# Kernel tuning notes

Measured on AMD Instinct MI355X. Metric: run time of the kernel, lower is better.

## Reference

```python
import jax, jax.numpy as jnp
import numpy as np

EPS = 1e-6
B, C, D = 128, 1000, 1024


def setup_inputs() -> dict:
    key = jax.random.key(0)
    k1, k2, k3, k4 = jax.random.split(key, 4)
    x = jax.random.normal(k1, (B, D), dtype=jnp.float32)
    # xavier-normal-ish prototypes
    mu = jax.random.normal(k2, (C, D), dtype=jnp.float32) * (2.0 / (C + D)) ** 0.5
    beta = jax.random.normal(k3, (D,), dtype=jnp.float32) * 0.1
    # L initialized as identity + small lower-triangular noise (full_sigma=True)
    L = jnp.eye(D, dtype=jnp.float32) + jnp.tril(
        jax.random.normal(k4, (D, D), dtype=jnp.float32) * 0.01)
    lmbda = jnp.asarray(0.1, dtype=jnp.float32)
    scale = jnp.asarray(10.0, dtype=jnp.float32)
    return {"x": x, "mu": mu, "beta": beta, "L": L, "lmbda": lmbda, "scale": scale}


def reference(x, mu, beta, L, lmbda, scale):
    # Sigma = tril(L) @ tril(L)^T + eps*I  (positive definite)
    Lt = jnp.tril(L)
    sigma = Lt @ Lt.T + EPS * jnp.eye(L.shape[0], dtype=L.dtype)
    # diff: [B, C, D]
    diff = x[:, None, :] - mu[None, :, :]
    # quadratic form v^T Sigma v per (b, c): contract once, then reduce
    ds = jnp.einsum('bcd,df->bcf', diff, sigma)   # [B, C, D]
    quad = jnp.sum(ds * diff, axis=-1)            # [B, C]
    beta_dot = jnp.einsum('d,bcd->bc', beta, diff)  # [B, C]
    riemannian = jnp.sqrt(quad + EPS)
    directional = lmbda * jnp.sqrt(beta_dot * beta_dot + EPS)  # smooth |.|
    return -scale * (riemannian + directional)
```

## Files before the change

### kernel.cpp

```cpp
#include <hip/hip_runtime.h>

#define D_DIM 1024
#define B_DIM 128
#define C_DIM 1000
#define M_ALL 1152
#define EPSF 1e-6f

typedef __attribute__((ext_vector_type(8))) short short8;
typedef __attribute__((ext_vector_type(4))) float f32x4;

static __device__ __forceinline__ unsigned short f2bf(float f) {
    union { float f; unsigned int u; } v; v.f = f;
    unsigned int u = v.u;
    u += 0x7fffu + ((u >> 16) & 1u);
    return (unsigned short)(u >> 16);
}


__global__ __launch_bounds__(256)
void pack_all(const float* __restrict__ x, const float* __restrict__ mu,
              const float* __restrict__ beta, const float* __restrict__ L,
              unsigned short* __restrict__ A_frag, unsigned short* __restrict__ LT_frag,
              float* __restrict__ nrm, float* __restrict__ bdot) {
    __shared__ __align__(16) unsigned short s_tile[64 * 72];
    __shared__ float red[2][4];
    const int tid = threadIdx.x, bid = blockIdx.x;

    if (bid < M_ALL) {
        const int m = bid;
        float4 v;
        if (m < B_DIM)              v = *(const float4*)(x + m * D_DIM + tid * 4);
        else if (m < B_DIM + C_DIM) v = *(const float4*)(mu + (m - B_DIM) * D_DIM + tid * 4);
        else                        v = make_float4(0.f, 0.f, 0.f, 0.f);
        ushort4 o;
        o.x = f2bf(v.x); o.y = f2bf(v.y); o.z = f2bf(v.z); o.w = f2bf(v.w);
        int mtile = m >> 4, kc = tid >> 3, qk = (tid >> 1) & 3, jj = (tid & 1) * 4;
        *(ushort4*)(A_frag + (mtile * 32 + kc) * 512 + (qk * 16 + (m & 15)) * 8 + jj) = o;

        float4 bt4 = *(const float4*)(beta + tid * 4);
        float sa = v.x*v.x + v.y*v.y + v.z*v.z + v.w*v.w;
        float sb = bt4.x*v.x + bt4.y*v.y + bt4.z*v.z + bt4.w*v.w;
#pragma unroll
        for (int off = 32; off > 0; off >>= 1) {
            sa += __shfl_down(sa, off);
            sb += __shfl_down(sb, off);
        }
        int lane = tid & 63, wv = tid >> 6;
        if (lane == 0) { red[0][wv] = sa; red[1][wv] = sb; }
        __syncthreads();
        if (tid == 0) {
            nrm[m]  = EPSF * (red[0][0] + red[0][1] + red[0][2] + red[0][3]);
            bdot[m] = red[1][0] + red[1][1] + red[1][2] + red[1][3];
        }
    } else {
        const int t = bid - M_ALL;
        const int k0 = (t >> 4) * 64, n0 = (t & 15) * 64;
        const int tn = tid & 63, tq = tid >> 6;
#pragma unroll
        for (int i = 0; i < 16; ++i) {
            int kk = tq + i * 4;
            int k = k0 + kk, n = n0 + tn;
            float v = (k >= n) ? L[k * D_DIM + n] : 0.f;
            s_tile[tn * 72 + kk] = f2bf(v);
        }
        __syncthreads();
        const int p = tid >> 5, s = tid & 31;
        const int np = p >> 1, kc2 = p & 1;
        const int ntile = (n0 >> 4) + np, kcg = (k0 >> 5) + kc2;
#pragma unroll
        for (int e = 0; e < 2; ++e) {
            int l = s * 2 + e;
            int lq = l >> 4, nr = l & 15;
            short8 vv = *(const short8*)&s_tile[(np * 16 + nr) * 72 + kc2 * 32 + lq * 8];
            *(short8*)(LT_frag + (ntile * 32 + kcg) * 512 + l * 8) = vv;
        }
    }
}

__global__ __launch_bounds__(256)
void gemm_p(const unsigned short* __restrict__ A_frag,
            const unsigned short* __restrict__ LT_frag,
            unsigned short* __restrict__ P_frag, float* __restrict__ nrm) {
    __shared__ __align__(16) unsigned short s_resh[4 * 1024];
    const int wv = threadIdx.x >> 6, lane = threadIdx.x & 63;
    const int wid = blockIdx.x * 4 + wv;
    const int lrow = lane & 15, q = lane >> 4;
    const int mt = wid >> 5, nt = wid & 31;
    const unsigned short* Ab0 = A_frag  + ((2 * mt) * 32) * 512 + lane * 8;
    const unsigned short* Ab1 = Ab0 + 32 * 512;
    const unsigned short* Bb0 = LT_frag + ((2 * nt) * 32) * 512 + lane * 8;
    const unsigned short* Bb1 = Bb0 + 32 * 512;

    f32x4 acc[2][2] = {};
#pragma unroll 4
    for (int kc = nt; kc < 32; ++kc) {
        short8 a0 = *(const short8*)(Ab0 + kc * 512);
        short8 a1 = *(const short8*)(Ab1 + kc * 512);
        short8 b0 = *(const short8*)(Bb0 + kc * 512);
        short8 b1 = *(const short8*)(Bb1 + kc * 512);
        acc[0][0] = __builtin_amdgcn_mfma_f32_16x16x32_bf16(a0, b0, acc[0][0], 0, 0, 0);
        acc[0][1] = __builtin_amdgcn_mfma_f32_16x16x32_bf16(a0, b1, acc[0][1], 0, 0, 0);
        acc[1][0] = __builtin_amdgcn_mfma_f32_16x16x32_bf16(a1, b0, acc[1][0], 0, 0, 0);
        acc[1][1] = __builtin_amdgcn_mfma_f32_16x16x32_bf16(a1, b1, acc[1][1], 0, 0, 0);
    }

#pragma unroll
    for (int mi = 0; mi < 2; ++mi)
#pragma unroll
    for (int r = 0; r < 4; ++r) {
        float s = acc[mi][0][r] * acc[mi][0][r] + acc[mi][1][r] * acc[mi][1][r];
#pragma unroll
        for (int off = 1; off < 16; off <<= 1) s += __shfl_xor(s, off);
        if (lrow == 0) atomicAdd(&nrm[mt * 32 + mi * 16 + q * 4 + r], s);
    }
    unsigned short* wls = s_resh + wv * 1024;
#pragma unroll
    for (int mi = 0; mi < 2; ++mi)
#pragma unroll
    for (int ni = 0; ni < 2; ++ni) {
        int lp = (ni * 2 + (lrow >> 3)) * 16 + q * 4;
#pragma unroll
        for (int r = 0; r < 4; ++r)
            wls[mi * 512 + (lp + r) * 8 + (lrow & 7)] = f2bf(acc[mi][ni][r]);
    }
    asm volatile("s_waitcnt lgkmcnt(0)" ::: "memory");
#pragma unroll
    for (int mi = 0; mi < 2; ++mi) {
        short8 vv = *(const short8*)(wls + mi * 512 + lane * 8);
        *(short8*)(P_frag + ((2 * mt + mi) * 32 + nt) * 512 + lane * 8) = vv;
    }
}

__global__ __launch_bounds__(256)
void gemm_cross(const unsigned short* __restrict__ P_frag,
                const float* __restrict__ nrm, const float* __restrict__ bdot,
                const float* __restrict__ lmbda_p, const float* __restrict__ scale_p,
                float* __restrict__ out) {
    const int wid  = blockIdx.x * 4 + (threadIdx.x >> 6);
    const int lane = threadIdx.x & 63;
    const int lrow = lane & 15, q = lane >> 4;
    const int bt = wid / 63, ct = wid % 63;
    const unsigned short* up = P_frag + (bt * 32) * 512 + lane * 8;
    const unsigned short* vp = P_frag + ((8 + ct) * 32) * 512 + lane * 8;

    f32x4 acc = {};
#pragma unroll 8
    for (int kc = 0; kc < 32; ++kc) {
        short8 a = *(const short8*)(up + kc * 512);
        short8 b = *(const short8*)(vp + kc * 512);
        acc = __builtin_amdgcn_mfma_f32_16x16x32_bf16(a, b, acc, 0, 0, 0);
    }
    const float lm = *lmbda_p, sc = *scale_p;
    const int c = ct * 16 + lrow;
    if (c < C_DIM) {
        float nm = nrm[B_DIM + c], bm = bdot[B_DIM + c];
#pragma unroll
        for (int r = 0; r < 4; ++r) {
            int b = bt * 16 + q * 4 + r;
            float quad = nrm[b] + nm - 2.f * acc[r] + EPSF;
            quad = fmaxf(quad, 0.f);
            float bd = bdot[b] - bm;
            out[b * C_DIM + c] = -sc * (sqrtf(quad) + lm * sqrtf(fmaf(bd, bd, EPSF)));
        }
    }
}

extern "C" void kernel_launch(void* const* d_in, const int* in_sizes, int n_in,
                              void* d_out, int out_size, void* d_ws, size_t ws_size,
                              hipStream_t stream) {
    const float* x     = (const float*)d_in[0];
    const float* mu    = (const float*)d_in[1];
    const float* beta  = (const float*)d_in[2];
    const float* L     = (const float*)d_in[3];
    const float* lmbda = (const float*)d_in[4];
    const float* scale = (const float*)d_in[5];
    float* out = (float*)d_out;

    char* ws = (char*)d_ws;
    unsigned short* A_frag  = (unsigned short*)ws;
    unsigned short* LT_frag = (unsigned short*)(ws + 2359296);
    unsigned short* P_frag  = (unsigned short*)(ws + 2359296 + 2097152);
    float* fws  = (float*)(ws + 2359296 + 2097152 + 2359296);
    float* nrm  = fws;
    float* bdot = fws + M_ALL;

    dim3 blk(256);
    pack_all  <<<M_ALL + 256, blk, 0, stream>>>(x, mu, beta, L, A_frag, LT_frag, nrm, bdot);
    gemm_p    <<<288, blk, 0, stream>>>(A_frag, LT_frag, P_frag, nrm);
    gemm_cross<<<126, blk, 0, stream>>>(P_frag, nrm, bdot, lmbda, scale, out);
}
```

Baseline: 98.79 us.

## Fuse bf16 packing into the L-projection GEMM and compute row norms in cross GEMM

Removes the separate pack kernel: the projection GEMM now loads fp32 x/mu and L directly, converts them to bf16 into shared-memory tiles (masking L to lower-triangular), and computes eps-norms and beta dots in the nt==0 blocks. Projected-row squared norms are no longer accumulated with atomics; the cross GEMM recomputes them from the bf16 fragments it already loads. This saves one launch and the intermediate fragment round-trip through global memory, but the tiled GEMM has no software pipelining and nt==0 blocks do extra work, and norms now come from bf16-rounded values.

```diff
diff --git a/kernel.cpp b/kernel.cpp
--- a/kernel.cpp
+++ b/kernel.cpp
@@ -15,105 +15,84 @@
     u += 0x7fffu + ((u >> 16) & 1u);
     return (unsigned short)(u >> 16);
 }
+static __device__ __forceinline__ float bf2f(unsigned short s) {
+    union { unsigned int u; float f; } v; v.u = ((unsigned int)s) << 16;
+    return v.f;
+}
 
 
 __global__ __launch_bounds__(256)
-void pack_all(const float* __restrict__ x, const float* __restrict__ mu,
-              const float* __restrict__ beta, const float* __restrict__ L,
-              unsigned short* __restrict__ A_frag, unsigned short* __restrict__ LT_frag,
-              float* __restrict__ nrm, float* __restrict__ bdot) {
-    __shared__ __align__(16) unsigned short s_tile[64 * 72];
-    __shared__ float red[2][4];
-    const int tid = threadIdx.x, bid = blockIdx.x;
+void gemm_uv(const float* __restrict__ x, const float* __restrict__ mu,
+             const float* __restrict__ beta, const float* __restrict__ L,
+             unsigned short* __restrict__ uv_frag,
+             float* __restrict__ eps_nrm, float* __restrict__ bdot) {
+    __shared__ __align__(16) unsigned short As[64][72];
+    __shared__ __align__(16) unsigned short Bs[64][72];
+    __shared__ __align__(16) unsigned short wls_all[4096];
+    const int tid = threadIdx.x;
+    const int nt = blockIdx.x, mt = blockIdx.y;
+    const int m0 = mt * 64, n0 = nt * 64;
+    const int wv = tid >> 6, lane = tid & 63;
+    const int lrow = lane & 15, q = lane >> 4;
+    const int wm = (wv & 1) * 32, wn = (wv >> 1) * 32;
 
-    if (bid < M_ALL) {
-        const int m = bid;
-        float4 v;
-        if (m < B_DIM)              v = *(const float4*)(x + m * D_DIM + tid * 4);
-        else if (m < B_DIM + C_DIM) v = *(const float4*)(mu + (m - B_DIM) * D_DIM + tid * 4);
-        else                        v = make_float4(0.f, 0.f, 0.f, 0.f);
-        ushort4 o;
-        o.x = f2bf(v.x); o.y = f2bf(v.y); o.z = f2bf(v.z); o.w = f2bf(v.w);
-        int mtile = m >> 4, kc = tid >> 3, qk = (tid >> 1) & 3, jj = (tid & 1) * 4;
-        *(ushort4*)(A_frag + (mtile * 32 + kc) * 512 + (qk * 16 + (m & 15)) * 8 + jj) = o;
+    const int am = tid >> 2, aks = (tid & 3) * 16;
+    const int bn4 = (tid & 15) * 4, bkl = tid >> 4;
+    const int m_abs = m0 + am;
+    const float* arow = (m_abs < B_DIM) ? (x + m_abs * D_DIM)
+                      : (m_abs < B_DIM + C_DIM) ? (mu + (m_abs - B_DIM) * D_DIM)
+                      : (const float*)0;
 
-        float4 bt4 = *(const float4*)(beta + tid * 4);
-        float sa = v.x*v.x + v.y*v.y + v.z*v.z + v.w*v.w;
-        float sb = bt4.x*v.x + bt4.y*v.y + bt4.z*v.z + bt4.w*v.w;
+    float sa = 0.f, sb = 0.f;
+    f32x4 acc[2][2] = {};
+
+    for (int k0 = n0; k0 < D_DIM; k0 += 64) {
 #pragma unroll
-        for (int off = 32; off > 0; off >>= 1) {
-            sa += __shfl_down(sa, off);
-            sb += __shfl_down(sb, off);
+        for (int i = 0; i < 4; ++i) {
+            int k = aks + i * 4;
+            float4 v = arow ? *(const float4*)(arow + k0 + k)
+                            : make_float4(0.f, 0.f, 0.f, 0.f);
+            ushort4 o;
+            o.x = f2bf(v.x); o.y = f2bf(v.y); o.z = f2bf(v.z); o.w = f2bf(v.w);
+            *(ushort4*)&As[am][k] = o;
+            if (nt == 0) {
+                sa += v.x * v.x + v.y * v.y + v.z * v.z + v.w * v.w;
+                float4 bb = *(const float4*)(beta + k0 + k);
+                sb += bb.x * v.x + bb.y * v.y + bb.z * v.z + bb.w * v.w;
+            }
         }
-        int lane = tid & 63, wv = tid >> 6;
-        if (lane == 0) { red[0][wv] = sa; red[1][wv] = sb; }
-        __syncthreads();
-        if (tid == 0) {
-            nrm[m]  = EPSF * (red[0][0] + red[0][1] + red[0][2] + red[0][3]);
-            bdot[m] = red[1][0] + red[1][1] + red[1][2] + red[1][3];
-        }
-    } else {
-        const int t = bid - M_ALL;
-        const int k0 = (t >> 4) * 64, n0 = (t & 15) * 64;
-        const int tn = tid & 63, tq = tid >> 6;
 #pragma unroll
-        for (int i = 0; i < 16; ++i) {
-            int kk = tq + i * 4;
-            int k = k0 + kk, n = n0 + tn;
-            float v = (k >= n) ? L[k * D_DIM + n] : 0.f;
-            s_tile[tn * 72 + kk] = f2bf(v);
+        for (int p = 0; p < 4; ++p) {
+            int kl = bkl + p * 16;
+            int k_abs = k0 + kl, nb = n0 + bn4;
+            float4 v = *(const float4*)(L + (size_t)k_abs * D_DIM + nb);
+            Bs[bn4 + 0][kl] = (k_abs >= nb + 0) ? f2bf(v.x) : (unsigned short)0;
+            Bs[bn4 + 1][kl] = (k_abs >= nb + 1) ? f2bf(v.y) : (unsigned short)0;
+            Bs[bn4 + 2][kl] = (k_abs >= nb + 2) ? f2bf(v.z) : (unsigned short)0;
+            Bs[bn4 + 3][kl] = (k_abs >= nb + 3) ? f2bf(v.w) : (unsigned short)0;
         }
         __syncthreads();
-        const int p = tid >> 5, s = tid & 31;
-        const int np = p >> 1, kc2 = p & 1;
-        const int ntile = (n0 >> 4) + np, kcg = (k0 >> 5) + kc2;
 #pragma unroll
-        for (int e = 0; e < 2; ++e) {
-            int l = s * 2 + e;
-            int lq = l >> 4, nr = l & 15;
-            short8 vv = *(const short8*)&s_tile[(np * 16 + nr) * 72 + kc2 * 32 + lq * 8];
-            *(short8*)(LT_frag + (ntile * 32 + kcg) * 512 + l * 8) = vv;
+        for (int ks = 0; ks < 64; ks += 32) {
+            short8 a0 = *(const short8*)&As[wm + lrow][ks + q * 8];
+            short8 a1 = *(const short8*)&As[wm + 16 + lrow][ks + q * 8];
+            short8 b0 = *(const short8*)&Bs[wn + lrow][ks + q * 8];
+            short8 b1 = *(const short8*)&Bs[wn + 16 + lrow][ks + q * 8];
+            acc[0][0] = __builtin_amdgcn_mfma_f32_16x16x32_bf16(a0, b0, acc[0][0], 0, 0, 0);
+            acc[0][1] = __builtin_amdgcn_mfma_f32_16x16x32_bf16(a0, b1, acc[0][1], 0, 0, 0);
+            acc[1][0] = __builtin_amdgcn_mfma_f32_16x16x32_bf16(a1, b0, acc[1][0], 0, 0, 0);
+            acc[1][1] = __builtin_amdgcn_mfma_f32_16x16x32_bf16(a1, b1, acc[1][1], 0, 0, 0);
         }
-    }
-}
-
-__global__ __launch_bounds__(256)
-void gemm_p(const unsigned short* __restrict__ A_frag,
-            const unsigned short* __restrict__ LT_frag,
-            unsigned short* __restrict__ P_frag, float* __restrict__ nrm) {
-    __shared__ __align__(16) unsigned short s_resh[4 * 1024];
-    const int wv = threadIdx.x >> 6, lane = threadIdx.x & 63;
-    const int wid = blockIdx.x * 4 + wv;
-    const int lrow = lane & 15, q = lane >> 4;
-    const int mt = wid >> 5, nt = wid & 31;
-    const unsigned short* Ab0 = A_frag  + ((2 * mt) * 32) * 512 + lane * 8;
-    const unsigned short* Ab1 = Ab0 + 32 * 512;
-    const unsigned short* Bb0 = LT_frag + ((2 * nt) * 32) * 512 + lane * 8;
-    const unsigned short* Bb1 = Bb0 + 32 * 512;
-
-    f32x4 acc[2][2] = {};
-#pragma unroll 4
-    for (int kc = nt; kc < 32; ++kc) {
-        short8 a0 = *(const short8*)(Ab0 + kc * 512);
-        short8 a1 = *(const short8*)(Ab1 + kc * 512);
-        short8 b0 = *(const short8*)(Bb0 + kc * 512);
-        short8 b1 = *(const short8*)(Bb1 + kc * 512);
-        acc[0][0] = __builtin_amdgcn_mfma_f32_16x16x32_bf16(a0, b0, acc[0][0], 0, 0, 0);
-        acc[0][1] = __builtin_amdgcn_mfma_f32_16x16x32_bf16(a0, b1, acc[0][1], 0, 0, 0);
-        acc[1][0] = __builtin_amdgcn_mfma_f32_16x16x32_bf16(a1, b0, acc[1][0], 0, 0, 0);
-        acc[1][1] = __builtin_amdgcn_mfma_f32_16x16x32_bf16(a1, b1, acc[1][1], 0, 0, 0);
+        __syncthreads();
     }
 
-#pragma unroll
-    for (int mi = 0; mi < 2; ++mi)
-#pragma unroll
-    for (int r = 0; r < 4; ++r) {
-        float s = acc[mi][0][r] * acc[mi][0][r] + acc[mi][1][r] * acc[mi][1][r];
-#pragma unroll
-        for (int off = 1; off < 16; off <<= 1) s += __shfl_xor(s, off);
-        if (lrow == 0) atomicAdd(&nrm[mt * 32 + mi * 16 + q * 4 + r], s);
+    if (nt == 0) {
+        sa += __shfl_down(sa, 2); sa += __shfl_down(sa, 1);
+        sb += __shfl_down(sb, 2); sb += __shfl_down(sb, 1);
+        if ((tid & 3) == 0) { eps_nrm[m_abs] = EPSF * sa; bdot[m_abs] = sb; }
     }
-    unsigned short* wls = s_resh + wv * 1024;
+
+    unsigned short* wls = wls_all + wv * 1024;
 #pragma unroll
     for (int mi = 0; mi < 2; ++mi)
 #pragma unroll
@@ -124,40 +103,57 @@
             wls[mi * 512 + (lp + r) * 8 + (lrow & 7)] = f2bf(acc[mi][ni][r]);
     }
     asm volatile("s_waitcnt lgkmcnt(0)" ::: "memory");
+    const int mt32 = (m0 + wm) >> 5, kc = (n0 + wn) >> 5;
 #pragma unroll
     for (int mi = 0; mi < 2; ++mi) {
         short8 vv = *(const short8*)(wls + mi * 512 + lane * 8);
-        *(short8*)(P_frag + ((2 * mt + mi) * 32 + nt) * 512 + lane * 8) = vv;
+        *(short8*)(uv_frag + ((2 * mt32 + mi) * 32 + kc) * 512 + lane * 8) = vv;
     }
 }
 
 __global__ __launch_bounds__(256)
-void gemm_cross(const unsigned short* __restrict__ P_frag,
-                const float* __restrict__ nrm, const float* __restrict__ bdot,
+void gemm_cross(const unsigned short* __restrict__ uv_frag,
+                const float* __restrict__ eps_nrm, const float* __restrict__ bdot,
                 const float* __restrict__ lmbda_p, const float* __restrict__ scale_p,
                 float* __restrict__ out) {
     const int wid  = blockIdx.x * 4 + (threadIdx.x >> 6);
     const int lane = threadIdx.x & 63;
     const int lrow = lane & 15, q = lane >> 4;
     const int bt = wid / 63, ct = wid % 63;
-    const unsigned short* up = P_frag + (bt * 32) * 512 + lane * 8;
-    const unsigned short* vp = P_frag + ((8 + ct) * 32) * 512 + lane * 8;
+    const unsigned short* up = uv_frag + (bt * 32) * 512 + lane * 8;
+    const unsigned short* vp = uv_frag + ((8 + ct) * 32) * 512 + lane * 8;
 
     f32x4 acc = {};
+    float su = 0.f, sv = 0.f;
 #pragma unroll 8
     for (int kc = 0; kc < 32; ++kc) {
         short8 a = *(const short8*)(up + kc * 512);
         short8 b = *(const short8*)(vp + kc * 512);
         acc = __builtin_amdgcn_mfma_f32_16x16x32_bf16(a, b, acc, 0, 0, 0);
+#pragma unroll
+        for (int j = 0; j < 8; ++j) {
+            float fa = bf2f((unsigned short)a[j]);
+            float fb = bf2f((unsigned short)b[j]);
+            su = fmaf(fa, fa, su);
+            sv = fmaf(fb, fb, sv);
+        }
     }
+    su += __shfl_xor(su, 16); su += __shfl_xor(su, 32);
+    sv += __shfl_xor(sv, 16); sv += __shfl_xor(sv, 32);
+
+    float nu_r[4];
+#pragma unroll
+    for (int r = 0; r < 4; ++r) nu_r[r] = __shfl(su, q * 4 + r);
+
     const float lm = *lmbda_p, sc = *scale_p;
     const int c = ct * 16 + lrow;
     if (c < C_DIM) {
-        float nm = nrm[B_DIM + c], bm = bdot[B_DIM + c];
+        float base_c = sv + eps_nrm[B_DIM + c];
+        float bm = bdot[B_DIM + c];
 #pragma unroll
         for (int r = 0; r < 4; ++r) {
             int b = bt * 16 + q * 4 + r;
-            float quad = nrm[b] + nm - 2.f * acc[r] + EPSF;
+            float quad = nu_r[r] + base_c - 2.f * acc[r] + eps_nrm[b] + EPSF;
             quad = fmaxf(quad, 0.f);
             float bd = bdot[b] - bm;
             out[b * C_DIM + c] = -sc * (sqrtf(quad) + lm * sqrtf(fmaf(bd, bd, EPSF)));
@@ -177,15 +173,10 @@
     float* out = (float*)d_out;
 
     char* ws = (char*)d_ws;
-    unsigned short* A_frag  = (unsigned short*)ws;
-    unsigned short* LT_frag = (unsigned short*)(ws + 2359296);
-    unsigned short* P_frag  = (unsigned short*)(ws + 2359296 + 2097152);
-    float* fws  = (float*)(ws + 2359296 + 2097152 + 2359296);
-    float* nrm  = fws;
-    float* bdot = fws + M_ALL;
+    unsigned short* uv_frag = (unsigned short*)ws;
+    float* eps_nrm = (float*)(ws + 2359296);
+    float* bdot    = (float*)(ws + 2359296 + 4608);
 
-    dim3 blk(256);
-    pack_all  <<<M_ALL + 256, blk, 0, stream>>>(x, mu, beta, L, A_frag, LT_frag, nrm, bdot);
-    gemm_p    <<<288, blk, 0, stream>>>(A_frag, LT_frag, P_frag, nrm);
-    gemm_cross<<<126, blk, 0, stream>>>(P_frag, nrm, bdot, lmbda, scale, out);
+    gemm_uv   <<<dim3(16, 18), 256, 0, stream>>>(x, mu, beta, L, uv_frag, eps_nrm, bdot);
+    gemm_cross<<<126, 256, 0, stream>>>(uv_frag, eps_nrm, bdot, lmbda, scale, out);
 }
```

Result: slower. 125.8 us (+27.4%).

## Pack 8 rows per block and split-K the cross GEMM across two waves

Applied to the files above, without the earlier changes.

The pack kernel now handles eight rows per block, one 32-lane group per row, looping over K. This replaces one 256-thread block per row and drops the LDS reduction and barrier. The cross GEMM splits K between two waves per output tile and combines the partial sums through shared memory, doubling the grid to 252 blocks to raise parallelism on the many CUs. It also raises the gemm_p unroll and adds size_t index casts; the split-K path adds a barrier and an LDS round trip.

```diff
diff --git a/kernel.cpp b/kernel.cpp
--- a/kernel.cpp
+++ b/kernel.cpp
@@ -23,44 +23,45 @@
               unsigned short* __restrict__ A_frag, unsigned short* __restrict__ LT_frag,
               float* __restrict__ nrm, float* __restrict__ bdot) {
     __shared__ __align__(16) unsigned short s_tile[64 * 72];
-    __shared__ float red[2][4];
     const int tid = threadIdx.x, bid = blockIdx.x;
 
-    if (bid < M_ALL) {
-        const int m = bid;
-        float4 v;
-        if (m < B_DIM)              v = *(const float4*)(x + m * D_DIM + tid * 4);
-        else if (m < B_DIM + C_DIM) v = *(const float4*)(mu + (m - B_DIM) * D_DIM + tid * 4);
-        else                        v = make_float4(0.f, 0.f, 0.f, 0.f);
-        ushort4 o;
-        o.x = f2bf(v.x); o.y = f2bf(v.y); o.z = f2bf(v.z); o.w = f2bf(v.w);
-        int mtile = m >> 4, kc = tid >> 3, qk = (tid >> 1) & 3, jj = (tid & 1) * 4;
-        *(ushort4*)(A_frag + (mtile * 32 + kc) * 512 + (qk * 16 + (m & 15)) * 8 + jj) = o;
-
-        float4 bt4 = *(const float4*)(beta + tid * 4);
-        float sa = v.x*v.x + v.y*v.y + v.z*v.z + v.w*v.w;
-        float sb = bt4.x*v.x + bt4.y*v.y + bt4.z*v.z + bt4.w*v.w;
-#pragma unroll
-        for (int off = 32; off > 0; off >>= 1) {
+    if (bid < 144) {
+        const int m = bid * 8 + (tid >> 5);
+        const int cg = tid & 31;
+        const float* arow = (m < B_DIM) ? (x + (size_t)m * D_DIM)
+                          : (m < B_DIM + C_DIM) ? (mu + (size_t)(m - B_DIM) * D_DIM)
+                          : (const float*)0;
+        const int mtile = m >> 4, rl = m & 15;
+        const int qk = (cg & 7) >> 1, jj = (cg & 1) * 4;
+        float sa = 0.f, sb = 0.f;
+#pragma unroll
+        for (int pass = 0; pass < 8; ++pass) {
+            int k = cg * 4 + pass * 128;
+            float4 v = arow ? *(const float4*)(arow + k)
+                            : make_float4(0.f, 0.f, 0.f, 0.f);
+            ushort4 o;
+            o.x = f2bf(v.x); o.y = f2bf(v.y); o.z = f2bf(v.z); o.w = f2bf(v.w);
+            int kc = (cg >> 3) + pass * 4;
+            *(ushort4*)(A_frag + ((size_t)(mtile * 32 + kc)) * 512 + (qk * 16 + rl) * 8 + jj) = o;
+            float4 bb = *(const float4*)(beta + k);
+            sa += v.x * v.x + v.y * v.y + v.z * v.z + v.w * v.w;
+            sb += bb.x * v.x + bb.y * v.y + bb.z * v.z + bb.w * v.w;
+        }
+#pragma unroll
+        for (int off = 16; off > 0; off >>= 1) {
             sa += __shfl_down(sa, off);
             sb += __shfl_down(sb, off);
         }
-        int lane = tid & 63, wv = tid >> 6;
-        if (lane == 0) { red[0][wv] = sa; red[1][wv] = sb; }
-        __syncthreads();
-        if (tid == 0) {
-            nrm[m]  = EPSF * (red[0][0] + red[0][1] + red[0][2] + red[0][3]);
-            bdot[m] = red[1][0] + red[1][1] + red[1][2] + red[1][3];
-        }
+        if (cg == 0) { nrm[m] = EPSF * sa; bdot[m] = sb; }
     } else {
-        const int t = bid - M_ALL;
+        const int t = bid - 144;
         const int k0 = (t >> 4) * 64, n0 = (t & 15) * 64;
         const int tn = tid & 63, tq = tid >> 6;
 #pragma unroll
         for (int i = 0; i < 16; ++i) {
             int kk = tq + i * 4;
             int k = k0 + kk, n = n0 + tn;
-            float v = (k >= n) ? L[k * D_DIM + n] : 0.f;
+            float v = (k >= n) ? L[(size_t)k * D_DIM + n] : 0.f;
             s_tile[tn * 72 + kk] = f2bf(v);
         }
         __syncthreads();
@@ -72,7 +73,7 @@
             int l = s * 2 + e;
             int lq = l >> 4, nr = l & 15;
             short8 vv = *(const short8*)&s_tile[(np * 16 + nr) * 72 + kc2 * 32 + lq * 8];
-            *(short8*)(LT_frag + (ntile * 32 + kcg) * 512 + l * 8) = vv;
+            *(short8*)(LT_frag + ((size_t)(ntile * 32 + kcg)) * 512 + l * 8) = vv;
         }
     }
 }
@@ -86,13 +87,13 @@
     const int wid = blockIdx.x * 4 + wv;
     const int lrow = lane & 15, q = lane >> 4;
     const int mt = wid >> 5, nt = wid & 31;
-    const unsigned short* Ab0 = A_frag  + ((2 * mt) * 32) * 512 + lane * 8;
+    const unsigned short* Ab0 = A_frag  + ((size_t)(2 * mt) * 32) * 512 + lane * 8;
     const unsigned short* Ab1 = Ab0 + 32 * 512;
-    const unsigned short* Bb0 = LT_frag + ((2 * nt) * 32) * 512 + lane * 8;
+    const unsigned short* Bb0 = LT_frag + ((size_t)(2 * nt) * 32) * 512 + lane * 8;
     const unsigned short* Bb1 = Bb0 + 32 * 512;
 
     f32x4 acc[2][2] = {};
-#pragma unroll 4
+#pragma unroll 8
     for (int kc = nt; kc < 32; ++kc) {
         short8 a0 = *(const short8*)(Ab0 + kc * 512);
         short8 a1 = *(const short8*)(Ab1 + kc * 512);
@@ -127,7 +128,7 @@
 #pragma unroll
     for (int mi = 0; mi < 2; ++mi) {
         short8 vv = *(const short8*)(wls + mi * 512 + lane * 8);
-        *(short8*)(P_frag + ((2 * mt + mi) * 32 + nt) * 512 + lane * 8) = vv;
+        *(short8*)(P_frag + ((size_t)((2 * mt + mi) * 32 + nt)) * 512 + lane * 8) = vv;
     }
 }
 
@@ -136,20 +137,28 @@
                 const float* __restrict__ nrm, const float* __restrict__ bdot,
                 const float* __restrict__ lmbda_p, const float* __restrict__ scale_p,
                 float* __restrict__ out) {
-    const int wid  = blockIdx.x * 4 + (threadIdx.x >> 6);
-    const int lane = threadIdx.x & 63;
+    __shared__ f32x4 red[2][64];
+    const int wv = threadIdx.x >> 6, lane = threadIdx.x & 63;
+    const int tile = blockIdx.x * 2 + (wv >> 1);
+    const int kh = wv & 1;
     const int lrow = lane & 15, q = lane >> 4;
-    const int bt = wid / 63, ct = wid % 63;
-    const unsigned short* up = P_frag + (bt * 32) * 512 + lane * 8;
-    const unsigned short* vp = P_frag + ((8 + ct) * 32) * 512 + lane * 8;
+    const int bt = tile / 63, ct = tile % 63;
+    const unsigned short* up = P_frag + ((size_t)(bt * 32 + kh * 16)) * 512 + lane * 8;
+    const unsigned short* vp = P_frag + ((size_t)((8 + ct) * 32 + kh * 16)) * 512 + lane * 8;
 
     f32x4 acc = {};
 #pragma unroll 8
-    for (int kc = 0; kc < 32; ++kc) {
+    for (int kc = 0; kc < 16; ++kc) {
         short8 a = *(const short8*)(up + kc * 512);
         short8 b = *(const short8*)(vp + kc * 512);
         acc = __builtin_amdgcn_mfma_f32_16x16x32_bf16(a, b, acc, 0, 0, 0);
     }
+    if (kh == 1) red[wv >> 1][lane] = acc;
+    __syncthreads();
+    if (kh == 1) return;
+    f32x4 o = red[wv >> 1][lane];
+    acc[0] += o[0]; acc[1] += o[1]; acc[2] += o[2]; acc[3] += o[3];
+
     const float lm = *lmbda_p, sc = *scale_p;
     const int c = ct * 16 + lrow;
     if (c < C_DIM) {
@@ -185,7 +194,7 @@
     float* bdot = fws + M_ALL;
 
     dim3 blk(256);
-    pack_all  <<<M_ALL + 256, blk, 0, stream>>>(x, mu, beta, L, A_frag, LT_frag, nrm, bdot);
+    pack_all  <<<400, blk, 0, stream>>>(x, mu, beta, L, A_frag, LT_frag, nrm, bdot);
     gemm_p    <<<288, blk, 0, stream>>>(A_frag, LT_frag, P_frag, nrm);
-    gemm_cross<<<126, blk, 0, stream>>>(P_frag, nrm, bdot, lmbda, scale, out);
-}
+    gemm_cross<<<252, blk, 0, stream>>>(P_frag, nrm, bdot, lmbda, scale, out);
+}
```

Measured after the change: 95.56 us. 1.03x faster.
